# Kernel tuning notes

Hardware: AMD Instinct MI355X
Metric: run time of the kernel (lower is better)

## Reference

```python
import jax, jax.numpy as jnp
import numpy as np
import math

D_MODEL = 1024
N_HEADS = 16
D_HEAD = D_MODEL // N_HEADS


def setup_inputs() -> dict:
    key = jax.random.key(0)
    ks = jax.random.split(key, 5)
    scale = 1.0 / math.sqrt(D_MODEL)
    x = jax.random.normal(ks[0], (4, 2048, D_MODEL), dtype=jnp.float32)
    W_q = jax.random.uniform(ks[1], (D_MODEL, D_MODEL), jnp.float32, -scale, scale)
    W_k = jax.random.uniform(ks[2], (D_MODEL, D_MODEL), jnp.float32, -scale, scale)
    W_v = jax.random.uniform(ks[3], (D_MODEL, D_MODEL), jnp.float32, -scale, scale)
    W_o = jax.random.uniform(ks[4], (D_MODEL, D_MODEL), jnp.float32, -scale, scale)
    return {"x": x, "W_q": W_q, "W_k": W_k, "W_v": W_v, "W_o": W_o}


def reference(x, W_q, W_k, W_v, W_o):
    B, S, D = x.shape
    H, Dh = N_HEADS, D_HEAD
    # nn.Linear(bias=False): y = x @ W.T
    q = (x @ W_q.T).reshape(B, S, H, Dh).transpose(0, 2, 1, 3)  # [B,H,S,Dh]
    k = (x @ W_k.T).reshape(B, S, H, Dh).transpose(0, 2, 1, 3)
    v = (x @ W_v.T).reshape(B, S, H, Dh).transpose(0, 2, 1, 3)
    scores = jnp.einsum('bhqd,bhkd->bhqk', q, k) / math.sqrt(Dh)  # [B,H,S,S]
    causal = jnp.triu(jnp.ones((S, S), dtype=bool), k=1)
    scores = jnp.where(causal, jnp.float32(-1e9), scores)
    attn = jax.nn.softmax(scores, axis=-1)  # dropout = identity (eval)
    out = jnp.einsum('bhqk,bhkd->bhqd', attn, v)  # [B,H,S,Dh]
    out = out.transpose(0, 2, 1, 3).reshape(B, S, D)
    return out @ W_o.T
```

## Files before the change

kernel.cpp:

```cpp
#include <hip/hip_runtime.h>
#include <hip/hip_bf16.h>

typedef __attribute__((ext_vector_type(8))) short short8;
typedef __attribute__((ext_vector_type(4))) float f32x4;
typedef __attribute__((ext_vector_type(16))) float f32x16;
typedef __attribute__((ext_vector_type(4))) unsigned short u16x4;

#define S_LEN 2048
#define DH 64
#define NH 16
#define SCALE_LOG2 0.18033688011112042f
#define EXP2F(x) __builtin_amdgcn_exp2f(x)
#define GLOAD_LDS16(src, dst)                                             \
  __builtin_amdgcn_global_load_lds(                                       \
      (const __attribute__((address_space(1))) void*)(src),               \
      (__attribute__((address_space(3))) void*)(dst), 16, 0, 0)

__device__ __forceinline__ unsigned short f2bf(float f) {
  unsigned int u = __float_as_uint(f);
  u += 0x7fffu + ((u >> 16) & 1u);
  return (unsigned short)(u >> 16);
}

__device__ __forceinline__ unsigned int cvtpk(float a, float b) {
  unsigned int r;
  asm("v_cvt_pk_bf16_f32 %0, %1, %2" : "=v"(r) : "v"(a), "v"(b));
  return r;
}
__device__ __forceinline__ void plswap(unsigned int& a, unsigned int& b) {
  asm("v_permlane32_swap_b32 %0, %1" : "+v"(a), "+v"(b));
}

__device__ __forceinline__ int swz8c(int row, int chunk) {
  return row * 64 + ((chunk ^ (row & 7)) << 3);
}

__global__ void convert_all(const float* __restrict__ x,
                            const float* __restrict__ w0,
                            const float* __restrict__ w1,
                            const float* __restrict__ w2,
                            const float* __restrict__ w3,
                            unsigned short* __restrict__ xb,
                            unsigned short* __restrict__ o0,
                            unsigned short* __restrict__ o1,
                            unsigned short* __restrict__ o2,
                            unsigned short* __restrict__ o3) {
  const int bid = blockIdx.x;
  const float* in;
  unsigned short* out;
  int i;
  if (bid < 8192) {
    in = x; out = xb;
    i = (bid * 256 + threadIdx.x) * 4;
  } else {
    const int seg = (bid - 8192) >> 10;
    in  = (seg == 0) ? w0 : (seg == 1) ? w1 : (seg == 2) ? w2 : w3;
    out = (seg == 0) ? o0 : (seg == 1) ? o1 : (seg == 2) ? o2 : o3;
    i = (((bid - 8192) & 1023) * 256 + threadIdx.x) * 4;
  }
  float4 v = *reinterpret_cast<const float4*>(in + i);
  u16x4 o;
  o.x = f2bf(v.x); o.y = f2bf(v.y); o.z = f2bf(v.z); o.w = f2bf(v.w);
  *reinterpret_cast<u16x4*>(out + i) = o;
}

template <int MODE>
__global__ __launch_bounds__(256) void gemm_bt(
    const unsigned short* __restrict__ A,
    const unsigned short* __restrict__ B,
    void* __restrict__ out, int M, int N, int K) {
  __shared__ __align__(16) unsigned short As[2][128 * 64];
  __shared__ __align__(16) unsigned short Bs[2][128 * 64];
  const int tid = threadIdx.x;
  const int l = tid & 63, w = tid >> 6;
  const int wr = w >> 1, wc = w & 1;
  const int g = l >> 4, c = l & 15;
  const int m0 = blockIdx.x * 128;
  const int n0 = blockIdx.y * 128;
  const int sr8 = l >> 3;
  const int scol = ((l & 7) ^ sr8) * 8;

  f32x4 acc[4][4] = {};

#define GSTAGE(buf, k0)                                                     \
  do {                                                                      \
    _Pragma("unroll") for (int p = 0; p < 4; ++p) {                         \
      int r0 = w * 32 + p * 8;                                              \
      GLOAD_LDS16(&A[(long)(m0 + r0 + sr8) * K + (k0) + scol],              \
                  &As[buf][r0 * 64]);                                       \
      GLOAD_LDS16(&B[(long)(n0 + r0 + sr8) * K + (k0) + scol],              \
                  &Bs[buf][r0 * 64]);                                       \
    }                                                                       \
  } while (0)

  GSTAGE(0, 0);
  __syncthreads();

  int cur = 0;
  for (int k0 = 0; k0 < K; k0 += 64) {
    if (k0 + 64 < K) GSTAGE(cur ^ 1, k0 + 64);
#pragma unroll
    for (int s = 0; s < 2; ++s) {
      short8 af[4], bf[4];
#pragma unroll
      for (int m = 0; m < 4; ++m)
        af[m] = *reinterpret_cast<const short8*>(
            &As[cur][swz8c(wr * 64 + m * 16 + c, s * 4 + g)]);
#pragma unroll
      for (int n = 0; n < 4; ++n)
        bf[n] = *reinterpret_cast<const short8*>(
            &Bs[cur][swz8c(wc * 64 + n * 16 + c, s * 4 + g)]);
      __builtin_amdgcn_s_setprio(1);
#pragma unroll
      for (int m = 0; m < 4; ++m)
#pragma unroll
        for (int n = 0; n < 4; ++n)
          acc[m][n] = __builtin_amdgcn_mfma_f32_16x16x32_bf16(
              af[m], bf[n], acc[m][n], 0, 0, 0);
      __builtin_amdgcn_s_setprio(0);
    }
    __syncthreads();
    cur ^= 1;
  }
#undef GSTAGE

#pragma unroll
  for (int m = 0; m < 4; ++m) {
#pragma unroll
    for (int n = 0; n < 4; ++n) {
#pragma unroll
      for (int r = 0; r < 4; ++r) {
        int row = m0 + wr * 64 + m * 16 + g * 4 + r;
        int col = n0 + wc * 64 + n * 16 + c;
        float v = acc[m][n][r];
        if (MODE == 3) {
          reinterpret_cast<float*>(out)[(long)row * N + col] = v;
        } else if (MODE == 2) {
          int b = row >> 11, s = row & 2047;
          int h = col >> 6, d = col & 63;
          reinterpret_cast<unsigned short*>(
              out)[((long)((b * NH + h) * DH + d)) * S_LEN + s] = f2bf(v);
        } else {
          if (MODE == 1) v *= SCALE_LOG2;
          int b = row >> 11, s = row & 2047;
          int h = col >> 6, d = col & 63;
          reinterpret_cast<unsigned short*>(
              out)[((long)((b * NH + h) * S_LEN + s)) * DH + d] = f2bf(v);
        }
      }
    }
  }
}

__global__ __launch_bounds__(256) void attn_fwd(
    const unsigned short* __restrict__ Q, const unsigned short* __restrict__ Kg,
    const unsigned short* __restrict__ Vt, unsigned short* __restrict__ O) {
  __shared__ __align__(16) unsigned short Ks[2][64 * 64];
  __shared__ __align__(16) unsigned short Vs[2][64 * 64];

  const int tid = threadIdx.x;
  const int l = tid & 63, w = tid >> 6;
  const int ln = l & 31, hi = l >> 5, hi4 = hi * 4;
  const int bh = blockIdx.x;
  const int qb = 15 - blockIdx.y;
  const int b = bh >> 4, h = bh & 15;
  const long base = (long)bh * (S_LEN * DH);
  const int sr8 = l >> 3;
  const int scol = ((l & 7) ^ sr8) * 8;
  const int q0w = qb * 128 + w * 32;

  short8 qf[4];
  {
    const unsigned short* qp = Q + base + (long)(q0w + ln) * DH + hi * 8;
#pragma unroll
    for (int ks = 0; ks < 4; ++ks)
      qf[ks] = *reinterpret_cast<const short8*>(qp + ks * 16);
  }

  f32x16 o0 = {}, o1 = {};
  float l_r = 0.f;
  const int ntb = qb * 2 + 2;
  const int ntw = q0w / 64 + 1;

#pragma unroll
  for (int p = 0; p < 2; ++p) {
    int r0 = w * 16 + p * 8;
    GLOAD_LDS16(&Kg[base + (long)(r0 + sr8) * DH + scol], &Ks[0][r0 * 64]);
    GLOAD_LDS16(&Vt[base + (long)(r0 + sr8) * S_LEN + scol], &Vs[0][r0 * 64]);
  }
  __syncthreads();

  int cur = 0;
  for (int t = 0; t < ntb; ++t) {
    if (t + 1 < ntb) {
      const int kv1 = (t + 1) * 64;
#pragma unroll
      for (int p = 0; p < 2; ++p) {
        int r0 = w * 16 + p * 8;
        GLOAD_LDS16(&Kg[base + (long)(kv1 + r0 + sr8) * DH + scol],
                    &Ks[cur ^ 1][r0 * 64]);
        GLOAD_LDS16(&Vt[base + (long)(r0 + sr8) * S_LEN + kv1 + scol],
                    &Vs[cur ^ 1][r0 * 64]);
      }
    }
    if (t < ntw) {
      const unsigned short* ksb = Ks[cur];
      const unsigned short* vsb = Vs[cur];
      const int kv0 = t * 64;

      f32x16 s0 = {}, s1 = {};
      __builtin_amdgcn_s_setprio(1);
#pragma unroll
      for (int ks = 0; ks < 4; ++ks) {
        short8 ak0 =
            *reinterpret_cast<const short8*>(&ksb[swz8c(ln, ks * 2 + hi)]);
        short8 ak1 = *reinterpret_cast<const short8*>(
            &ksb[swz8c(32 + ln, ks * 2 + hi)]);
        s0 = __builtin_amdgcn_mfma_f32_32x32x16_bf16(ak0, qf[ks], s0, 0, 0, 0);
        s1 = __builtin_amdgcn_mfma_f32_32x32x16_bf16(ak1, qf[ks], s1, 0, 0, 0);
      }
      __builtin_amdgcn_s_setprio(0);

      if (t == ntw - 1) {
        const int qrel = (q0w - kv0) + ln;
#pragma unroll
        for (int r = 0; r < 16; ++r) {
          const int rowv = (r & 3) + 8 * (r >> 2) + hi4;
          if (rowv > qrel) s0[r] = -1e30f;
          if (rowv + 32 > qrel) s1[r] = -1e30f;
        }
      }

      float a0 = 0.f, a1 = 0.f, a2 = 0.f, a3 = 0.f;
#pragma unroll
      for (int r = 0; r < 16; r += 4) {
        s0[r] = EXP2F(s0[r]);         s0[r + 1] = EXP2F(s0[r + 1]);
        s0[r + 2] = EXP2F(s0[r + 2]); s0[r + 3] = EXP2F(s0[r + 3]);
        s1[r] = EXP2F(s1[r]);         s1[r + 1] = EXP2F(s1[r + 1]);
        s1[r + 2] = EXP2F(s1[r + 2]); s1[r + 3] = EXP2F(s1[r + 3]);
        a0 += s0[r] + s1[r];
        a1 += s0[r + 1] + s1[r + 1];
        a2 += s0[r + 2] + s1[r + 2];
        a3 += s0[r + 3] + s1[r + 3];
      }
      l_r += (a0 + a1) + (a2 + a3);

      __builtin_amdgcn_s_setprio(1);
#pragma unroll
      for (int ks = 0; ks < 4; ++ks) {
        unsigned int wa, wb, wc2, wd;
        if (ks == 0) {
          wa = cvtpk(s0[0], s0[1]);   wc2 = cvtpk(s0[2], s0[3]);
          wb = cvtpk(s0[4], s0[5]);   wd  = cvtpk(s0[6], s0[7]);
        } else if (ks == 1) {
          wa = cvtpk(s0[8], s0[9]);   wc2 = cvtpk(s0[10], s0[11]);
          wb = cvtpk(s0[12], s0[13]); wd  = cvtpk(s0[14], s0[15]);
        } else if (ks == 2) {
          wa = cvtpk(s1[0], s1[1]);   wc2 = cvtpk(s1[2], s1[3]);
          wb = cvtpk(s1[4], s1[5]);   wd  = cvtpk(s1[6], s1[7]);
        } else {
          wa = cvtpk(s1[8], s1[9]);   wc2 = cvtpk(s1[10], s1[11]);
          wb = cvtpk(s1[12], s1[13]); wd  = cvtpk(s1[14], s1[15]);
        }
        plswap(wa, wb);
        plswap(wc2, wd);
        union { unsigned int u[4]; short8 s; } pa;
        pa.u[0] = wa; pa.u[1] = wc2; pa.u[2] = wb; pa.u[3] = wd;
        short8 v0 =
            *reinterpret_cast<const short8*>(&vsb[swz8c(ln, ks * 2 + hi)]);
        short8 v1 = *reinterpret_cast<const short8*>(
            &vsb[swz8c(32 + ln, ks * 2 + hi)]);
        o0 = __builtin_amdgcn_mfma_f32_32x32x16_bf16(pa.s, v0, o0, 0, 0, 0);
        o1 = __builtin_amdgcn_mfma_f32_32x32x16_bf16(pa.s, v1, o1, 0, 0, 0);
      }
      __builtin_amdgcn_s_setprio(0);
    }
    __syncthreads();
    cur ^= 1;
  }

  l_r += __shfl_xor(l_r, 32, 64);
  float inv = 1.0f / l_r;
#pragma unroll
  for (int r = 0; r < 16; ++r) {
    const int rowv = (r & 3) + 8 * (r >> 2) + hi4;
    float iv = __shfl(inv, rowv, 64);
    int q = q0w + rowv;
    long ob = ((long)(b * S_LEN + q)) * 1024 + h * 64 + ln;
    O[ob] = f2bf(o0[r] * iv);
    O[ob + 32] = f2bf(o1[r] * iv);
  }
}

extern "C" void kernel_launch(void* const* d_in, const int* in_sizes, int n_in,
                              void* d_out, int out_size, void* d_ws,
                              size_t ws_size, hipStream_t stream) {
  const float* x  = (const float*)d_in[0];
  const float* Wq = (const float*)d_in[1];
  const float* Wk = (const float*)d_in[2];
  const float* Wv = (const float*)d_in[3];
  const float* Wo = (const float*)d_in[4];
  float* out = (float*)d_out;
  char* ws = (char*)d_ws;

  unsigned short* xb  = (unsigned short*)(ws);
  unsigned short* Wqb = (unsigned short*)(ws + (16u << 20));
  unsigned short* Wkb = (unsigned short*)(ws + (18u << 20));
  unsigned short* Wvb = (unsigned short*)(ws + (20u << 20));
  unsigned short* Wob = (unsigned short*)(ws + (22u << 20));
  unsigned short* Vt  = (unsigned short*)(ws + (24u << 20));
  unsigned short* Ow  = (unsigned short*)(ws);
  unsigned short* Qw = (unsigned short*)d_out;
  unsigned short* Kw = (unsigned short*)d_out + (8u << 20);

  convert_all<<<12288, 256, 0, stream>>>(x, Wq, Wk, Wv, Wo, xb, Wqb, Wkb, Wvb,
                                         Wob);

  dim3 ggrid(64, 8);
  gemm_bt<1><<<ggrid, 256, 0, stream>>>(xb, Wqb, Qw, 8192, 1024, 1024);
  gemm_bt<0><<<ggrid, 256, 0, stream>>>(xb, Wkb, Kw, 8192, 1024, 1024);
  gemm_bt<2><<<ggrid, 256, 0, stream>>>(xb, Wvb, Vt, 8192, 1024, 1024);

  attn_fwd<<<dim3(64, 16), 256, 0, stream>>>(Qw, Kw, Vt, Ow);

  gemm_bt<3><<<ggrid, 256, 0, stream>>>(Ow, Wob, out, 8192, 1024, 1024);
}
```

Measured before the change: 160.6 us.

## Split attention KV range across two wave groups per block and merge partials

After: 164.4 us. 1.02x slower.

```diff
diff --git a/kernel.cpp b/kernel.cpp
--- a/kernel.cpp
+++ b/kernel.cpp
@@ -152,18 +152,20 @@
   }
 }
 
-__global__ __launch_bounds__(256) void attn_fwd(
+__global__ __launch_bounds__(512) void attn_fwd(
     const unsigned short* __restrict__ Q, const unsigned short* __restrict__ Kg,
     const unsigned short* __restrict__ Vt, unsigned short* __restrict__ O) {
-  __shared__ __align__(16) unsigned short Ks[2][64 * 64];
-  __shared__ __align__(16) unsigned short Vs[2][64 * 64];
+  __shared__ __align__(16) unsigned short Ks[2][2][64 * 64];
+  __shared__ __align__(16) unsigned short Vs[2][2][64 * 64];
+  __shared__ float mL[4][64];
 
   const int tid = threadIdx.x;
-  const int l = tid & 63, w = tid >> 6;
+  const int l = tid & 63, w8 = tid >> 6;
+  const int grp = w8 >> 2, w = w8 & 3;
   const int ln = l & 31, hi = l >> 5, hi4 = hi * 4;
   const int bh = blockIdx.x;
   const int qb = 15 - blockIdx.y;
-  const int b = bh >> 4, h = bh & 15;
+  const int b = bh >> 4, hd = bh & 15;
   const long base = (long)bh * (S_LEN * DH);
   const int sr8 = l >> 3;
   const int scol = ((l & 7) ^ sr8) * 8;
@@ -179,33 +181,32 @@
 
   f32x16 o0 = {}, o1 = {};
   float l_r = 0.f;
-  const int ntb = qb * 2 + 2;
+  const int HT = qb + 1;
+  const int t0 = grp * HT;
+  const int t1 = t0 + HT;
   const int ntw = q0w / 64 + 1;
 
-#pragma unroll
-  for (int p = 0; p < 2; ++p) {
-    int r0 = w * 16 + p * 8;
-    GLOAD_LDS16(&Kg[base + (long)(r0 + sr8) * DH + scol], &Ks[0][r0 * 64]);
-    GLOAD_LDS16(&Vt[base + (long)(r0 + sr8) * S_LEN + scol], &Vs[0][r0 * 64]);
-  }
+#define ASTAGE(buf, t)                                                      \
+  do {                                                                      \
+    const int _kv = (t) * 64;                                               \
+    _Pragma("unroll") for (int p = 0; p < 2; ++p) {                         \
+      int r0 = w * 16 + p * 8;                                              \
+      GLOAD_LDS16(&Kg[base + (long)(_kv + r0 + sr8) * DH + scol],           \
+                  &Ks[grp][buf][r0 * 64]);                                  \
+      GLOAD_LDS16(&Vt[base + (long)(r0 + sr8) * S_LEN + _kv + scol],        \
+                  &Vs[grp][buf][r0 * 64]);                                  \
+    }                                                                       \
+  } while (0)
+
+  ASTAGE(0, t0);
   __syncthreads();
 
   int cur = 0;
-  for (int t = 0; t < ntb; ++t) {
-    if (t + 1 < ntb) {
-      const int kv1 = (t + 1) * 64;
-#pragma unroll
-      for (int p = 0; p < 2; ++p) {
-        int r0 = w * 16 + p * 8;
-        GLOAD_LDS16(&Kg[base + (long)(kv1 + r0 + sr8) * DH + scol],
-                    &Ks[cur ^ 1][r0 * 64]);
-        GLOAD_LDS16(&Vt[base + (long)(r0 + sr8) * S_LEN + kv1 + scol],
-                    &Vs[cur ^ 1][r0 * 64]);
-      }
-    }
+  for (int t = t0; t < t1; ++t) {
+    if (t + 1 < t1) ASTAGE(cur ^ 1, t + 1);
     if (t < ntw) {
-      const unsigned short* ksb = Ks[cur];
-      const unsigned short* vsb = Vs[cur];
+      const unsigned short* ksb = Ks[grp][cur];
+      const unsigned short* vsb = Vs[grp][cur];
       const int kv0 = t * 64;
 
       f32x16 s0 = {}, s1 = {};
@@ -278,17 +279,41 @@
     __syncthreads();
     cur ^= 1;
   }
-
-  l_r += __shfl_xor(l_r, 32, 64);
-  float inv = 1.0f / l_r;
-#pragma unroll
-  for (int r = 0; r < 16; ++r) {
-    const int rowv = (r & 3) + 8 * (r >> 2) + hi4;
-    float iv = __shfl(inv, rowv, 64);
-    int q = q0w + rowv;
-    long ob = ((long)(b * S_LEN + q)) * 1024 + h * 64 + ln;
-    O[ob] = f2bf(o0[r] * iv);
-    O[ob + 32] = f2bf(o1[r] * iv);
+#undef ASTAGE
+
+  float* MB = (float*)&Ks[0][0][0];
+  const int mi = (w * 64 + l) * 16;
+  if (grp == 1) {
+#pragma unroll
+    for (int r = 0; r < 16; ++r) MB[mi + r] = o0[r];
+    mL[w][l] = l_r;
+  }
+  __syncthreads();
+  if (grp == 0) {
+#pragma unroll
+    for (int r = 0; r < 16; ++r) o0[r] += MB[mi + r];
+    l_r += mL[w][l];
+  }
+  __syncthreads();
+  if (grp == 1) {
+#pragma unroll
+    for (int r = 0; r < 16; ++r) MB[mi + r] = o1[r];
+  }
+  __syncthreads();
+  if (grp == 0) {
+#pragma unroll
+    for (int r = 0; r < 16; ++r) o1[r] += MB[mi + r];
+    l_r += __shfl_xor(l_r, 32, 64);
+    float inv = 1.0f / l_r;
+#pragma unroll
+    for (int r = 0; r < 16; ++r) {
+      const int rowv = (r & 3) + 8 * (r >> 2) + hi4;
+      float iv = __shfl(inv, rowv, 64);
+      int q = q0w + rowv;
+      long ob = ((long)(b * S_LEN + q)) * 1024 + hd * 64 + ln;
+      O[ob] = f2bf(o0[r] * iv);
+      O[ob + 32] = f2bf(o1[r] * iv);
+    }
   }
 }
 
@@ -321,7 +346,7 @@
   gemm_bt<0><<<ggrid, 256, 0, stream>>>(xb, Wkb, Kw, 8192, 1024, 1024);
   gemm_bt<2><<<ggrid, 256, 0, stream>>>(xb, Wvb, Vt, 8192, 1024, 1024);
 
-  attn_fwd<<<dim3(64, 16), 256, 0, stream>>>(Qw, Kw, Vt, Ow);
+  attn_fwd<<<dim3(64, 16), 512, 0, stream>>>(Qw, Kw, Vt, Ow);
 
   gemm_bt<3><<<ggrid, 256, 0, stream>>>(Ow, Wob, out, 8192, 1024, 1024);
 }
```

## Split KV range of longest causal query blocks and merge partial outputs

Applied to the files above, without the earlier changes.

Measured after the change: 167.9 us. 1.05x slower.

```diff
diff --git a/kernel.cpp b/kernel.cpp
--- a/kernel.cpp
+++ b/kernel.cpp
@@ -20,6 +20,9 @@
   unsigned int u = __float_as_uint(f);
   u += 0x7fffu + ((u >> 16) & 1u);
   return (unsigned short)(u >> 16);
+}
+__device__ __forceinline__ float bf2f(unsigned short u) {
+  return __uint_as_float((unsigned int)u << 16);
 }
 
 __device__ __forceinline__ unsigned int cvtpk(float a, float b) {
@@ -154,7 +157,9 @@
 
 __global__ __launch_bounds__(256) void attn_fwd(
     const unsigned short* __restrict__ Q, const unsigned short* __restrict__ Kg,
-    const unsigned short* __restrict__ Vt, unsigned short* __restrict__ O) {
+    const unsigned short* __restrict__ Vt, unsigned short* __restrict__ O,
+    unsigned short* __restrict__ H1, float* __restrict__ L0,
+    float* __restrict__ L1) {
   __shared__ __align__(16) unsigned short Ks[2][64 * 64];
   __shared__ __align__(16) unsigned short Vs[2][64 * 64];
 
@@ -162,8 +167,11 @@
   const int l = tid & 63, w = tid >> 6;
   const int ln = l & 31, hi = l >> 5, hi4 = hi * 4;
   const int bh = blockIdx.x;
-  const int qb = 15 - blockIdx.y;
-  const int b = bh >> 4, h = bh & 15;
+  const int y = blockIdx.y;
+  int qb, role;
+  if (y < 8) { qb = 15 - (y >> 1); role = 1 + (y & 1); }
+  else       { qb = 19 - y;        role = 0; }
+  const int b = bh >> 4, hd = bh & 15;
   const long base = (long)bh * (S_LEN * DH);
   const int sr8 = l >> 3;
   const int scol = ((l & 7) ^ sr8) * 8;
@@ -179,30 +187,28 @@
 
   f32x16 o0 = {}, o1 = {};
   float l_r = 0.f;
-  const int ntb = qb * 2 + 2;
+  const int t0 = (role == 2) ? qb + 1 : 0;
+  const int t1 = (role == 1) ? qb + 1 : 2 * qb + 2;
   const int ntw = q0w / 64 + 1;
 
-#pragma unroll
-  for (int p = 0; p < 2; ++p) {
-    int r0 = w * 16 + p * 8;
-    GLOAD_LDS16(&Kg[base + (long)(r0 + sr8) * DH + scol], &Ks[0][r0 * 64]);
-    GLOAD_LDS16(&Vt[base + (long)(r0 + sr8) * S_LEN + scol], &Vs[0][r0 * 64]);
-  }
+#define ASTAGE(buf, t)                                                      \
+  do {                                                                      \
+    const int _kv = (t) * 64;                                               \
+    _Pragma("unroll") for (int p = 0; p < 2; ++p) {                         \
+      int r0 = w * 16 + p * 8;                                              \
+      GLOAD_LDS16(&Kg[base + (long)(_kv + r0 + sr8) * DH + scol],           \
+                  &Ks[buf][r0 * 64]);                                       \
+      GLOAD_LDS16(&Vt[base + (long)(r0 + sr8) * S_LEN + _kv + scol],        \
+                  &Vs[buf][r0 * 64]);                                       \
+    }                                                                       \
+  } while (0)
+
+  ASTAGE(0, t0);
   __syncthreads();
 
   int cur = 0;
-  for (int t = 0; t < ntb; ++t) {
-    if (t + 1 < ntb) {
-      const int kv1 = (t + 1) * 64;
-#pragma unroll
-      for (int p = 0; p < 2; ++p) {
-        int r0 = w * 16 + p * 8;
-        GLOAD_LDS16(&Kg[base + (long)(kv1 + r0 + sr8) * DH + scol],
-                    &Ks[cur ^ 1][r0 * 64]);
-        GLOAD_LDS16(&Vt[base + (long)(r0 + sr8) * S_LEN + kv1 + scol],
-                    &Vs[cur ^ 1][r0 * 64]);
-      }
-    }
+  for (int t = t0; t < t1; ++t) {
+    if (t + 1 < t1) ASTAGE(cur ^ 1, t + 1);
     if (t < ntw) {
       const unsigned short* ksb = Ks[cur];
       const unsigned short* vsb = Vs[cur];
@@ -278,18 +284,66 @@
     __syncthreads();
     cur ^= 1;
   }
+#undef ASTAGE
 
   l_r += __shfl_xor(l_r, 32, 64);
-  float inv = 1.0f / l_r;
-#pragma unroll
-  for (int r = 0; r < 16; ++r) {
-    const int rowv = (r & 3) + 8 * (r >> 2) + hi4;
-    float iv = __shfl(inv, rowv, 64);
-    int q = q0w + rowv;
-    long ob = ((long)(b * S_LEN + q)) * 1024 + h * 64 + ln;
-    O[ob] = f2bf(o0[r] * iv);
-    O[ob + 32] = f2bf(o1[r] * iv);
-  }
+  if (role == 0) {
+    float inv = 1.0f / l_r;
+#pragma unroll
+    for (int r = 0; r < 16; ++r) {
+      const int rowv = (r & 3) + 8 * (r >> 2) + hi4;
+      float iv = __shfl(inv, rowv, 64);
+      int q = q0w + rowv;
+      long ob = ((long)(b * S_LEN + q)) * 1024 + hd * 64 + ln;
+      O[ob] = f2bf(o0[r] * iv);
+      O[ob + 32] = f2bf(o1[r] * iv);
+    }
+  } else if (role == 1) {
+#pragma unroll
+    for (int r = 0; r < 16; ++r) {
+      const int rowv = (r & 3) + 8 * (r >> 2) + hi4;
+      int q = q0w + rowv;
+      long ob = ((long)(b * S_LEN + q)) * 1024 + hd * 64 + ln;
+      O[ob] = f2bf(o0[r]);
+      O[ob + 32] = f2bf(o1[r]);
+    }
+    if (hi == 0) L0[(bh * 4 + (qb - 12)) * 128 + w * 32 + ln] = l_r;
+  } else {
+    unsigned short* hp =
+        H1 + ((long)((bh * 4 + (qb - 12)) * 128 + w * 32)) * 64;
+#pragma unroll
+    for (int r = 0; r < 16; ++r) {
+      const int rowv = (r & 3) + 8 * (r >> 2) + hi4;
+      hp[rowv * 64 + ln] = f2bf(o0[r]);
+      hp[rowv * 64 + ln + 32] = f2bf(o1[r]);
+    }
+    if (hi == 0) L1[(bh * 4 + (qb - 12)) * 128 + w * 32 + ln] = l_r;
+  }
+}
+
+__global__ void attn_merge(unsigned short* __restrict__ O,
+                           const unsigned short* __restrict__ H1,
+                           const float* __restrict__ L0,
+                           const float* __restrict__ L1) {
+  const int gid = blockIdx.x * 256 + threadIdx.x;
+  const int d4 = (gid & 15) * 4;
+  const int row = (gid >> 4) & 127;
+  const int qi = (gid >> 11) & 3;
+  const int bh = gid >> 13;
+  const int b = bh >> 4, hd = bh & 15;
+  const int q = (12 + qi) * 128 + row;
+  const long oidx = ((long)(b * S_LEN + q)) * 1024 + hd * 64 + d4;
+  const long hidx = ((long)((bh * 4 + qi) * 128 + row)) * 64 + d4;
+  const int lidx = (bh * 4 + qi) * 128 + row;
+  const float inv = 1.0f / (L0[lidx] + L1[lidx]);
+  u16x4 a = *reinterpret_cast<const u16x4*>(&O[oidx]);
+  u16x4 hh = *reinterpret_cast<const u16x4*>(&H1[hidx]);
+  u16x4 o;
+  o.x = f2bf((bf2f(a.x) + bf2f(hh.x)) * inv);
+  o.y = f2bf((bf2f(a.y) + bf2f(hh.y)) * inv);
+  o.z = f2bf((bf2f(a.z) + bf2f(hh.z)) * inv);
+  o.w = f2bf((bf2f(a.w) + bf2f(hh.w)) * inv);
+  *reinterpret_cast<u16x4*>(&O[oidx]) = o;
 }
 
 extern "C" void kernel_launch(void* const* d_in, const int* in_sizes, int n_in,
@@ -310,6 +364,9 @@
   unsigned short* Wob = (unsigned short*)(ws + (22u << 20));
   unsigned short* Vt  = (unsigned short*)(ws + (24u << 20));
   unsigned short* Ow  = (unsigned short*)(ws);
+  unsigned short* H1 = (unsigned short*)(ws + (16u << 20));
+  float* L0 = (float*)(ws + (20u << 20));
+  float* L1 = (float*)(ws + (20u << 20) + (128u << 10));
   unsigned short* Qw = (unsigned short*)d_out;
   unsigned short* Kw = (unsigned short*)d_out + (8u << 20);
 
@@ -321,7 +378,8 @@
   gemm_bt<0><<<ggrid, 256, 0, stream>>>(xb, Wkb, Kw, 8192, 1024, 1024);
   gemm_bt<2><<<ggrid, 256, 0, stream>>>(xb, Wvb, Vt, 8192, 1024, 1024);
 
-  attn_fwd<<<dim3(64, 16), 256, 0, stream>>>(Qw, Kw, Vt, Ow);
+  attn_fwd<<<dim3(64, 20), 256, 0, stream>>>(Qw, Kw, Vt, Ow, H1, L0, L1);
+  attn_merge<<<2048, 256, 0, stream>>>(Ow, H1, L0, L1);
 
   gemm_bt<3><<<ggrid, 256, 0, stream>>>(Ow, Wob, out, 8192, 1024, 1024);
 }
```
